# Kernel optimization log

Hardware: AMD Instinct MI355X
Metric: run time of the kernel (lower is better)

Reference implementation:

```python
import jax, jax.numpy as jnp
import numpy as np

B, S, E, H = 4, 4096, 768, 8
D = E // H  # head_dim = 96


def setup_inputs() -> dict:
    key = jax.random.key(0)
    ks = jax.random.split(key, 9)
    std = 1.0 / np.sqrt(E)
    return {
        "values": jax.random.normal(ks[0], (B, S, E), dtype=jnp.float32),
        "keys": jax.random.normal(ks[1], (B, S, E), dtype=jnp.float32),
        "query": jax.random.normal(ks[2], (B, S, E), dtype=jnp.float32),
        "mask": jax.random.randint(ks[3], (B, S, 1, 1), 0, 2, dtype=jnp.int32),
        "Wv": jax.random.normal(ks[4], (E, E), dtype=jnp.float32) * std,
        "Wk": jax.random.normal(ks[5], (E, E), dtype=jnp.float32) * std,
        "Wq": jax.random.normal(ks[6], (E, E), dtype=jnp.float32) * std,
        "Wo": jax.random.normal(ks[7], (E, E), dtype=jnp.float32) * std,
        "bo": jax.random.normal(ks[8], (E,), dtype=jnp.float32) * std,
    }


def reference(values, keys, query, mask, Wv, Wk, Wq, Wo, bo):
    b, s, e = query.shape
    h, d = H, e // H
    scale = e ** 0.5

    def split(x, W):
        # Linear (no bias) then view to [b, s, h, d] and permute to [b, h, s, d]
        return (x @ W.T).reshape(b, s, h, d).transpose(0, 2, 1, 3)

    v = split(values, Wv)   # [b, h, s, d]
    k = split(keys, Wk)     # [b, h, s, d]
    q = split(query, Wq)    # [b, h, s, d]

    # Faithful to torch.einsum('nqhd,nkhd->nhqk', q, k) with q,k laid out as
    # [b, h, s, d]: this contracts over d with s batched, producing a per-token
    # head-gram matrix att[b, s, i, j] = sum_d q[b,i,s,d] * k[b,j,s,d].
    att = jnp.einsum('bisd,bjsd->bsij', q, k)          # [b, s, h, h]
    att = jnp.where(mask == 0, jnp.float32(-1e20), att)
    att = jax.nn.softmax(att / scale, axis=3)

    # torch.einsum('nhql,nlhd->nqhd', att, v) with att [b,s,h,h], v [b,h,s,d]:
    # out[b, i, s, d] = sum_j att[b,s,i,j] * v[b,j,s,d]  -> [b, h, s, d]
    out = jnp.einsum('bsij,bjsd->bisd', att, v)        # [b, h, s, d]
    out = out.reshape(b, s, h * d)                      # row-major, matches torch .reshape
    return out @ Wo.T + bo
```

## Files before the change

### kernel.cpp

```cpp
#include <hip/hip_runtime.h>
#include <hip/hip_bf16.h>
#include <cstdint>


typedef unsigned short u16;
typedef short bf16x8 __attribute__((ext_vector_type(8)));
typedef float f32x4 __attribute__((ext_vector_type(4)));

#define B_  4
#define S_  4096
#define E_  768
#define H_  8
#define D_  96
#define T_  (B_*S_)
#define BM_ 128
#define BN_ 128
#define NT_ (E_/BN_)

static __device__ __forceinline__ u16 f2bf(float f) {
  unsigned u = __builtin_bit_cast(unsigned, f);
  u += 0x7fffu + ((u >> 16) & 1u);
  return (u16)(u >> 16);
}
static __device__ __forceinline__ unsigned pk2(float lo, float hi) {
  return (unsigned)f2bf(lo) | ((unsigned)f2bf(hi) << 16);
}
static __device__ __forceinline__ float bflo(unsigned u) {
  return __builtin_bit_cast(float, u << 16);
}
static __device__ __forceinline__ float bfhi(unsigned u) {
  return __builtin_bit_cast(float, u & 0xffff0000u);
}

__global__ __launch_bounds__(256) void conv_bf16(
    const float* __restrict__ src, u16* __restrict__ dst)
{
  const int i = blockIdx.x * 256 + threadIdx.x;
  const float4 v = ((const float4*)src)[i];
  uint2 w;
  w.x = pk2(v.x, v.y);
  w.y = pk2(v.z, v.w);
  ((uint2*)dst)[i] = w;
}

__global__ __launch_bounds__(256) void conv_w(
    const float* __restrict__ w0, const float* __restrict__ w1,
    const float* __restrict__ w2, const float* __restrict__ w3,
    u16* __restrict__ dst)
{
  const int bpw = (E_ * E_ / 4) / 256;
  const int which = blockIdx.x / bpw;
  const float* src = which == 0 ? w0 : which == 1 ? w1 : which == 2 ? w2 : w3;
  const int i = (blockIdx.x - which * bpw) * 256 + threadIdx.x;
  const float4 v = ((const float4*)src)[i];
  uint2 w;
  w.x = pk2(v.x, v.y);
  w.y = pk2(v.z, v.w);
  ((uint2*)(dst + (size_t)which * E_ * E_))[i] = w;
}

#define STAGE(BUF, KT)                                                         \
  {                                                                            \
    _Pragma("unroll")                                                          \
    for (int c = 0; c < 2; ++c) {                                              \
      const int idx = (c << 8) + tid;                                          \
      const int r = idx >> 2, g = idx & 3;                                     \
      const int gs = g ^ ((r >> 1) & 3);                                       \
      __builtin_amdgcn_global_load_lds(                                        \
          (const __attribute__((address_space(1))) void*)                     \
              (A + (size_t)(tM + r) * E_ + (KT) + (gs << 3)),                  \
          (__attribute__((address_space(3))) void*)                           \
              &lds[BUF][0][((c << 8) + (wave << 6)) << 3], 16, 0, 0);          \
      __builtin_amdgcn_global_load_lds(                                        \
          (const __attribute__((address_space(1))) void*)                     \
              (Wt + (size_t)(tN + r) * E_ + (KT) + (gs << 3)),                 \
          (__attribute__((address_space(3))) void*)                           \
              &lds[BUF][1][((c << 8) + (wave << 6)) << 3], 16, 0, 0);          \
    }                                                                          \
  }

#define LOADFRAGS(BUF)                                                         \
  {                                                                            \
    _Pragma("unroll")                                                          \
    for (int m = 0; m < 4; ++m)                                                \
      a[m] = *(const bf16x8*)&lds[BUF][0][((wr << 6) + (m << 4) + l15) * 32 + slotOff]; \
    _Pragma("unroll")                                                          \
    for (int n = 0; n < 4; ++n)                                                \
      b[n] = *(const bf16x8*)&lds[BUF][1][((wc << 6) + (n << 4) + l15) * 32 + slotOff]; \
  }

#define DOMFMA()                                                               \
  {                                                                            \
    _Pragma("unroll")                                                          \
    for (int m = 0; m < 4; ++m)                                                \
      _Pragma("unroll")                                                        \
      for (int n = 0; n < 4; ++n)                                              \
        acc[m][n] = __builtin_amdgcn_mfma_f32_16x16x32_bf16(a[m], b[n], acc[m][n], 0, 0, 0); \
  }

template<bool OUT_F32, bool BIAS>
__global__ __launch_bounds__(256, 3) void gemm_nt(
    const u16* __restrict__ A, const u16* __restrict__ Wt,
    const float* __restrict__ bias, void* __restrict__ Cv)
{
  __shared__ u16 lds[2][2][BM_ * 32];
  const int tid  = threadIdx.x;
  const int wave = tid >> 6;
  const int lane = tid & 63;
  const int wr = wave >> 1, wc = wave & 1;
  const int bid = blockIdx.x;
  const int wg  = (bid & 7) * (gridDim.x >> 3) + (bid >> 3);
  const int mT  = wg / NT_;
  const int nT  = wg - mT * NT_;
  const int tM = mT * BM_, tN = nT * BN_;
  const int l15 = lane & 15, l4 = lane >> 4;
  const int slotOff = (l4 ^ ((l15 >> 1) & 3)) << 3;

  f32x4 acc[4][4] = {};

  STAGE(0, 0);
  __syncthreads();

  for (int i = 0; i < 12; ++i) {
    const int kt = i << 6;
    {
      bf16x8 a[4], b[4];
      LOADFRAGS(0);
      STAGE(1, kt + 32);
      DOMFMA();
    }
    __syncthreads();
    {
      bf16x8 a[4], b[4];
      LOADFRAGS(1);
      if (i < 11) STAGE(0, kt + 64);
      DOMFMA();
    }
    __syncthreads();
  }

  if constexpr (OUT_F32) {
#pragma unroll
    for (int m = 0; m < 4; ++m) {
#pragma unroll
      for (int n = 0; n < 4; ++n) {
        const int row = tM + (wr << 6) + (m << 4) + (l4 << 2);
        const int col = tN + (wc << 6) + (n << 4) + l15;
        const float badd = BIAS ? bias[col] : 0.f;
#pragma unroll
        for (int r = 0; r < 4; ++r)
          ((float*)Cv)[(size_t)(row + r) * E_ + col] = acc[m][n][r] + badd;
      }
    }
  } else {
    __syncthreads();
    u16* lC = (u16*)lds;
#pragma unroll
    for (int m = 0; m < 4; ++m)
#pragma unroll
      for (int n = 0; n < 4; ++n) {
        const int row = (wr << 6) + (m << 4) + (l4 << 2);
        const int col = (wc << 6) + (n << 4) + l15;
#pragma unroll
        for (int r = 0; r < 4; ++r)
          lC[(row + r) * BN_ + col] = f2bf(acc[m][n][r]);
      }
    __syncthreads();
#pragma unroll
    for (int p = 0; p < 8; ++p) {
      const int row = (p << 4) + (wave << 2) + l4;
      const bf16x8 v = *(const bf16x8*)&lC[row * BN_ + (l15 << 3)];
      *(bf16x8*)((u16*)Cv + (size_t)(tM + row) * E_ + tN + (l15 << 3)) = v;
    }
  }
}

__global__ __launch_bounds__(256) void attn_tok(
    const u16* __restrict__ Q, const u16* __restrict__ K,
    const u16* __restrict__ V, const int* __restrict__ mask,
    u16* __restrict__ O)
{
  __shared__ float pl[4][8][8];
  const int tid = threadIdx.x, wave = tid >> 6, lane = tid & 63;
  const int t = blockIdx.x * 4 + wave;
  const int s = t & (S_ - 1);
  const int b = t >> 12;
  const int i = lane >> 3, j = lane & 7;

  const uint4* qp = (const uint4*)(Q + (size_t)t * E_ + i * D_);
  const uint4* kp = (const uint4*)(K + (size_t)t * E_ + j * D_);
  float acc = 0.f;
#pragma unroll
  for (int it = 0; it < 12; ++it) {
    const uint4 qv = qp[it], kv = kp[it];
    acc += bflo(qv.x) * bflo(kv.x) + bfhi(qv.x) * bfhi(kv.x);
    acc += bflo(qv.y) * bflo(kv.y) + bfhi(qv.y) * bfhi(kv.y);
    acc += bflo(qv.z) * bflo(kv.z) + bfhi(qv.z) * bfhi(kv.z);
    acc += bflo(qv.w) * bflo(kv.w) + bfhi(qv.w) * bfhi(kv.w);
  }
  float sv = (mask[t] == 0) ? -1e20f : acc;
  sv *= 0.03608439182435161f;
  float mx = sv;
  mx = fmaxf(mx, __shfl_xor(mx, 1));
  mx = fmaxf(mx, __shfl_xor(mx, 2));
  mx = fmaxf(mx, __shfl_xor(mx, 4));
  const float e = __expf(sv - mx);
  float sm = e;
  sm += __shfl_xor(sm, 1);
  sm += __shfl_xor(sm, 2);
  sm += __shfl_xor(sm, 4);
  pl[wave][i][j] = e / sm;
  __syncthreads();

  const int i2 = lane >> 3, db = lane & 7;
  float o[12] = {};
#pragma unroll
  for (int jj = 0; jj < 8; ++jj) {
    const float pj = pl[wave][i2][jj];
    const uint2* vp = (const uint2*)(V + (size_t)t * E_ + jj * D_ + db * 12);
    const uint2 v0 = vp[0], v1 = vp[1], v2 = vp[2];
    o[0]  += pj * bflo(v0.x);  o[1]  += pj * bfhi(v0.x);
    o[2]  += pj * bflo(v0.y);  o[3]  += pj * bfhi(v0.y);
    o[4]  += pj * bflo(v1.x);  o[5]  += pj * bfhi(v1.x);
    o[6]  += pj * bflo(v1.y);  o[7]  += pj * bfhi(v1.y);
    o[8]  += pj * bflo(v2.x);  o[9]  += pj * bfhi(v2.x);
    o[10] += pj * bflo(v2.y);  o[11] += pj * bfhi(v2.y);
  }
  const size_t row = (size_t)b * S_ + 512 * i2 + (s >> 3);
  u16* op = O + row * E_ + 96 * (s & 7) + db * 12;
  uint2 w0, w1, w2;
  w0.x = pk2(o[0], o[1]);
  w0.y = pk2(o[2], o[3]);
  w1.x = pk2(o[4], o[5]);
  w1.y = pk2(o[6], o[7]);
  w2.x = pk2(o[8], o[9]);
  w2.y = pk2(o[10], o[11]);
  ((uint2*)op)[0] = w0;
  ((uint2*)op)[1] = w1;
  ((uint2*)op)[2] = w2;
}

extern "C" void kernel_launch(void* const* d_in, const int* in_sizes, int n_in,
                              void* d_out, int out_size, void* d_ws, size_t ws_size,
                              hipStream_t stream)
{
  const float* values = (const float*)d_in[0];
  const float* keys   = (const float*)d_in[1];
  const float* query  = (const float*)d_in[2];
  const int*   mask   = (const int*)d_in[3];
  const float* Wv = (const float*)d_in[4];
  const float* Wk = (const float*)d_in[5];
  const float* Wq = (const float*)d_in[6];
  const float* Wo = (const float*)d_in[7];
  const float* bo = (const float*)d_in[8];

  const size_t TE = (size_t)T_ * E_;
  const size_t EE = (size_t)E_ * E_;
  u16* Qb = (u16*)d_ws;
  u16* Kb = Qb + TE;
  u16* Vb = Kb + TE;
  u16* Xt = Vb + TE;
  u16* Wb = Xt + TE;

  dim3 blk(256);
  dim3 gg(T_ / BM_ * NT_);
  dim3 gc(TE / 4 / 256);

  conv_w<<<dim3(4 * (E_ * E_ / 4) / 256), blk, 0, stream>>>(Wq, Wk, Wv, Wo, Wb);

  conv_bf16<<<gc, blk, 0, stream>>>(query, Xt);
  gemm_nt<false, false><<<gg, blk, 0, stream>>>(Xt, Wb + 0 * EE, nullptr, Qb);
  conv_bf16<<<gc, blk, 0, stream>>>(keys, Xt);
  gemm_nt<false, false><<<gg, blk, 0, stream>>>(Xt, Wb + 1 * EE, nullptr, Kb);
  conv_bf16<<<gc, blk, 0, stream>>>(values, Xt);
  gemm_nt<false, false><<<gg, blk, 0, stream>>>(Xt, Wb + 2 * EE, nullptr, Vb);

  attn_tok<<<dim3(T_ / 4), blk, 0, stream>>>(Qb, Kb, Vb, mask, Xt );

  gemm_nt<true, true><<<gg, blk, 0, stream>>>(Xt , Wb + 3 * EE, bo, (float*)d_out);
}
```

Measured before the change: 194.4 us.

## Fuse fp32-to-bf16 activation conversion into projection GEMM A-tile loading

Removes the three standalone conversion kernels and has the Q/K/V projection GEMMs read the fp32 activations directly. Each thread loads its fp32 values into registers, overlaps the loads with the MFMAs, and then packs them to bf16 with v_cvt_pk_bf16_f32 before writing them into swizzled LDS. This avoids writing and re-reading a bf16 copy of each input plus three extra launches. In exchange, the A tile is fetched at fp32 width through registers instead of via direct global-to-LDS loads, which raises register pressure and global traffic per tile and may change rounding behaviour on edge cases.

After: 227.2 us. 16.9% more time.

```diff
diff --git a/kernel.cpp b/kernel.cpp
--- a/kernel.cpp
+++ b/kernel.cpp
@@ -25,22 +25,16 @@
 static __device__ __forceinline__ unsigned pk2(float lo, float hi) {
   return (unsigned)f2bf(lo) | ((unsigned)f2bf(hi) << 16);
 }
+static __device__ __forceinline__ unsigned cvtpk(float lo, float hi) {
+  unsigned r;
+  asm("v_cvt_pk_bf16_f32 %0, %1, %2" : "=v"(r) : "v"(lo), "v"(hi));
+  return r;
+}
 static __device__ __forceinline__ float bflo(unsigned u) {
   return __builtin_bit_cast(float, u << 16);
 }
 static __device__ __forceinline__ float bfhi(unsigned u) {
   return __builtin_bit_cast(float, u & 0xffff0000u);
-}
-
-__global__ __launch_bounds__(256) void conv_bf16(
-    const float* __restrict__ src, u16* __restrict__ dst)
-{
-  const int i = blockIdx.x * 256 + threadIdx.x;
-  const float4 v = ((const float4*)src)[i];
-  uint2 w;
-  w.x = pk2(v.x, v.y);
-  w.y = pk2(v.z, v.w);
-  ((uint2*)dst)[i] = w;
 }
 
 __global__ __launch_bounds__(256) void conv_w(
@@ -59,7 +53,8 @@
   ((uint2*)(dst + (size_t)which * E_ * E_))[i] = w;
 }
 
-#define STAGE(BUF, KT)                                                         \
+
+#define STAGE_OP(BUF, OP, PTR, TBASE, KT)                                      \
   {                                                                            \
     _Pragma("unroll")                                                          \
     for (int c = 0; c < 2; ++c) {                                              \
@@ -68,15 +63,27 @@
       const int gs = g ^ ((r >> 1) & 3);                                       \
       __builtin_amdgcn_global_load_lds(                                        \
           (const __attribute__((address_space(1))) void*)                     \
-              (A + (size_t)(tM + r) * E_ + (KT) + (gs << 3)),                  \
+              ((PTR) + (size_t)((TBASE) + r) * E_ + (KT) + (gs << 3)),         \
           (__attribute__((address_space(3))) void*)                           \
-              &lds[BUF][0][((c << 8) + (wave << 6)) << 3], 16, 0, 0);          \
-      __builtin_amdgcn_global_load_lds(                                        \
-          (const __attribute__((address_space(1))) void*)                     \
-              (Wt + (size_t)(tN + r) * E_ + (KT) + (gs << 3)),                 \
-          (__attribute__((address_space(3))) void*)                           \
-              &lds[BUF][1][((c << 8) + (wave << 6)) << 3], 16, 0, 0);          \
+              &lds[BUF][OP][((c << 8) + (wave << 6)) << 3], 16, 0, 0);         \
     }                                                                          \
+  }
+
+#define LOAD_A(KT)                                                             \
+  const float4 av0 = *(const float4*)(agp + (KT));                             \
+  const float4 av1 = *(const float4*)(agp + (KT) + 4);                         \
+  const float4 av2 = *(const float4*)(agp + (KT) + 8);                         \
+  const float4 av3 = *(const float4*)(agp + (KT) + 12);
+
+#define WRITE_A(BUF)                                                           \
+  {                                                                            \
+    uint4 q0, q1;                                                              \
+    q0.x = cvtpk(av0.x, av0.y); q0.y = cvtpk(av0.z, av0.w);                    \
+    q0.z = cvtpk(av1.x, av1.y); q0.w = cvtpk(av1.z, av1.w);                    \
+    q1.x = cvtpk(av2.x, av2.y); q1.y = cvtpk(av2.z, av2.w);                    \
+    q1.z = cvtpk(av3.x, av3.y); q1.w = cvtpk(av3.z, av3.w);                    \
+    *(uint4*)&lds[BUF][0][ar * 32 + (((ah << 1) ^ aswz) << 3)] = q0;           \
+    *(uint4*)&lds[BUF][0][ar * 32 + ((((ah << 1) + 1) ^ aswz) << 3)] = q1;     \
   }
 
 #define LOADFRAGS(BUF)                                                         \
@@ -98,9 +105,9 @@
         acc[m][n] = __builtin_amdgcn_mfma_f32_16x16x32_bf16(a[m], b[n], acc[m][n], 0, 0, 0); \
   }
 
-template<bool OUT_F32, bool BIAS>
+template<bool A_F32, bool OUT_F32, bool BIAS>
 __global__ __launch_bounds__(256, 3) void gemm_nt(
-    const u16* __restrict__ A, const u16* __restrict__ Wt,
+    const void* __restrict__ Av, const u16* __restrict__ Wt,
     const float* __restrict__ bias, void* __restrict__ Cv)
 {
   __shared__ u16 lds[2][2][BM_ * 32];
@@ -116,9 +123,22 @@
   const int l15 = lane & 15, l4 = lane >> 4;
   const int slotOff = (l4 ^ ((l15 >> 1) & 3)) << 3;
 
+  const u16*   A16 = (const u16*)Av;
+  const float* A32 = (const float*)Av;
+  const int ar = tid >> 1, ah = tid & 1;
+  const int aswz = (ar >> 1) & 3;
+  const float* agp = A32 + (size_t)(tM + ar) * E_ + ah * 16;
+
   f32x4 acc[4][4] = {};
 
-  STAGE(0, 0);
+  if constexpr (A_F32) {
+    LOAD_A(0);
+    STAGE_OP(0, 1, Wt, tN, 0);
+    WRITE_A(0);
+  } else {
+    STAGE_OP(0, 0, A16, tM, 0);
+    STAGE_OP(0, 1, Wt, tN, 0);
+  }
   __syncthreads();
 
   for (int i = 0; i < 12; ++i) {
@@ -126,15 +146,35 @@
     {
       bf16x8 a[4], b[4];
       LOADFRAGS(0);
-      STAGE(1, kt + 32);
-      DOMFMA();
+      if constexpr (A_F32) {
+        LOAD_A(kt + 32);
+        STAGE_OP(1, 1, Wt, tN, kt + 32);
+        DOMFMA();
+        WRITE_A(1);
+      } else {
+        STAGE_OP(1, 0, A16, tM, kt + 32);
+        STAGE_OP(1, 1, Wt, tN, kt + 32);
+        DOMFMA();
+      }
     }
     __syncthreads();
     {
       bf16x8 a[4], b[4];
       LOADFRAGS(1);
-      if (i < 11) STAGE(0, kt + 64);
-      DOMFMA();
+      if (i < 11) {
+        if constexpr (A_F32) {
+          LOAD_A(kt + 64);
+          STAGE_OP(0, 1, Wt, tN, kt + 64);
+          DOMFMA();
+          WRITE_A(0);
+        } else {
+          STAGE_OP(0, 0, A16, tM, kt + 64);
+          STAGE_OP(0, 1, Wt, tN, kt + 64);
+          DOMFMA();
+        }
+      } else {
+        DOMFMA();
+      }
     }
     __syncthreads();
   }
@@ -259,23 +299,19 @@
   u16* Qb = (u16*)d_ws;
   u16* Kb = Qb + TE;
   u16* Vb = Kb + TE;
-  u16* Xt = Vb + TE;
-  u16* Wb = Xt + TE;
+  u16* O2 = Vb + TE;
+  u16* Wb = O2 + TE;
 
   dim3 blk(256);
   dim3 gg(T_ / BM_ * NT_);
-  dim3 gc(TE / 4 / 256);
 
   conv_w<<<dim3(4 * (E_ * E_ / 4) / 256), blk, 0, stream>>>(Wq, Wk, Wv, Wo, Wb);
 
-  conv_bf16<<<gc, blk, 0, stream>>>(query, Xt);
-  gemm_nt<false, false><<<gg, blk, 0, stream>>>(Xt, Wb + 0 * EE, nullptr, Qb);
-  conv_bf16<<<gc, blk, 0, stream>>>(keys, Xt);
-  gemm_nt<false, false><<<gg, blk, 0, stream>>>(Xt, Wb + 1 * EE, nullptr, Kb);
-  conv_bf16<<<gc, blk, 0, stream>>>(values, Xt);
-  gemm_nt<false, false><<<gg, blk, 0, stream>>>(Xt, Wb + 2 * EE, nullptr, Vb);
-
-  attn_tok<<<dim3(T_ / 4), blk, 0, stream>>>(Qb, Kb, Vb, mask, Xt );
-
-  gemm_nt<true, true><<<gg, blk, 0, stream>>>(Xt , Wb + 3 * EE, bo, (float*)d_out);
-}
+  gemm_nt<true, false, false><<<gg, blk, 0, stream>>>(query,  Wb + 0 * EE, nullptr, Qb);
+  gemm_nt<true, false, false><<<gg, blk, 0, stream>>>(keys,   Wb + 1 * EE, nullptr, Kb);
+  gemm_nt<true, false, false><<<gg, blk, 0, stream>>>(values, Wb + 2 * EE, nullptr, Vb);
+
+  attn_tok<<<dim3(T_ / 4), blk, 0, stream>>>(Qb, Kb, Vb, mask, O2);
+
+  gemm_nt<false, true, true><<<gg, blk, 0, stream>>>(O2, Wb + 3 * EE, bo, (float*)d_out);
+}
```

## Batch QKV conversions and projections into single launches with staggered start

Applied to the files above, without the earlier changes.

Merges the three input bf16 conversions into one kernel and the three Q/K/V projection GEMMs into one launch indexed by blockIdx.y, using the output buffer as scratch for the converted K and V inputs. This removes launch overhead and the serialization of small kernels, and gives the GPU a grid large enough to fill all CUs. It also adds an s_sleep-based stagger so blocks start at different times, which is meant to spread out memory traffic. The stagger adds idle delay at the start of each block, and the swizzle constant is hardcoded to 96.

Result: faster. 175.3 us (-9.8%).

```diff
diff --git a/kernel.cpp b/kernel.cpp
--- a/kernel.cpp
+++ b/kernel.cpp
@@ -32,17 +32,6 @@
   return __builtin_bit_cast(float, u & 0xffff0000u);
 }
 
-__global__ __launch_bounds__(256) void conv_bf16(
-    const float* __restrict__ src, u16* __restrict__ dst)
-{
-  const int i = blockIdx.x * 256 + threadIdx.x;
-  const float4 v = ((const float4*)src)[i];
-  uint2 w;
-  w.x = pk2(v.x, v.y);
-  w.y = pk2(v.z, v.w);
-  ((uint2*)dst)[i] = w;
-}
-
 __global__ __launch_bounds__(256) void conv_w(
     const float* __restrict__ w0, const float* __restrict__ w1,
     const float* __restrict__ w2, const float* __restrict__ w3,
@@ -59,6 +48,28 @@
   ((uint2*)(dst + (size_t)which * E_ * E_))[i] = w;
 }
 
+__global__ __launch_bounds__(256) void conv3(
+    const float* __restrict__ q, const float* __restrict__ k,
+    const float* __restrict__ v, u16* __restrict__ xq,
+    u16* __restrict__ xk, u16* __restrict__ xv)
+{
+  const int w = blockIdx.y;
+  const float* src = w == 0 ? q : w == 1 ? k : v;
+  u16* dst = w == 0 ? xq : w == 1 ? xk : xv;
+  const int i = blockIdx.x * 256 + threadIdx.x;
+  const float4 vv = ((const float4*)src)[i];
+  uint2 o;
+  o.x = pk2(vv.x, vv.y);
+  o.y = pk2(vv.z, vv.w);
+  ((uint2*)dst)[i] = o;
+}
+
+
+#define GLOAD(SRC, DST)                                                        \
+  __builtin_amdgcn_global_load_lds(                                            \
+      (const __attribute__((address_space(1))) void*)(SRC),                    \
+      (__attribute__((address_space(3))) void*)(DST), 16, 0, 0)
+
 #define STAGE(BUF, KT)                                                         \
   {                                                                            \
     _Pragma("unroll")                                                          \
@@ -66,16 +77,10 @@
       const int idx = (c << 8) + tid;                                          \
       const int r = idx >> 2, g = idx & 3;                                     \
       const int gs = g ^ ((r >> 1) & 3);                                       \
-      __builtin_amdgcn_global_load_lds(                                        \
-          (const __attribute__((address_space(1))) void*)                     \
-              (A + (size_t)(tM + r) * E_ + (KT) + (gs << 3)),                  \
-          (__attribute__((address_space(3))) void*)                           \
-              &lds[BUF][0][((c << 8) + (wave << 6)) << 3], 16, 0, 0);          \
-      __builtin_amdgcn_global_load_lds(                                        \
-          (const __attribute__((address_space(1))) void*)                     \
-              (Wt + (size_t)(tN + r) * E_ + (KT) + (gs << 3)),                 \
-          (__attribute__((address_space(3))) void*)                           \
-              &lds[BUF][1][((c << 8) + (wave << 6)) << 3], 16, 0, 0);          \
+      GLOAD(A + (size_t)(tM + r) * E_ + (KT) + (gs << 3),                      \
+            &lds[BUF][0][((c << 8) + (wave << 6)) << 3]);                      \
+      GLOAD(Wt + (size_t)(tN + r) * E_ + (KT) + (gs << 3),                     \
+            &lds[BUF][1][((c << 8) + (wave << 6)) << 3]);                      \
     }                                                                          \
   }
 
@@ -83,10 +88,10 @@
   {                                                                            \
     _Pragma("unroll")                                                          \
     for (int m = 0; m < 4; ++m)                                                \
-      a[m] = *(const bf16x8*)&lds[BUF][0][((wr << 6) + (m << 4) + l15) * 32 + slotOff]; \
+      a[m] = *(const bf16x8*)&lds[BUF][0][(((wr << 6) + (m << 4) + l15) << 5) + slotOff]; \
     _Pragma("unroll")                                                          \
     for (int n = 0; n < 4; ++n)                                                \
-      b[n] = *(const bf16x8*)&lds[BUF][1][((wc << 6) + (n << 4) + l15) * 32 + slotOff]; \
+      b[n] = *(const bf16x8*)&lds[BUF][1][(((wc << 6) + (n << 4) + l15) << 5) + slotOff]; \
   }
 
 #define DOMFMA()                                                               \
@@ -98,18 +103,39 @@
         acc[m][n] = __builtin_amdgcn_mfma_f32_16x16x32_bf16(a[m], b[n], acc[m][n], 0, 0, 0); \
   }
 
-template<bool OUT_F32, bool BIAS>
+template<bool BATCHED, bool OUT_F32, bool BIAS>
 __global__ __launch_bounds__(256, 3) void gemm_nt(
-    const u16* __restrict__ A, const u16* __restrict__ Wt,
-    const float* __restrict__ bias, void* __restrict__ Cv)
-{
-  __shared__ u16 lds[2][2][BM_ * 32];
+    const u16* __restrict__ a0, const u16* __restrict__ a1,
+    const u16* __restrict__ a2, const u16* __restrict__ Wall,
+    const float* __restrict__ bias,
+    void* __restrict__ c0, void* __restrict__ c1, void* __restrict__ c2)
+{
+  __shared__ u16 lds[2][2][4096];
+  const u16* A;
+  const u16* Wt;
+  void* Cv;
+  if constexpr (BATCHED) {
+    const int q_ = blockIdx.y;
+    A  = q_ == 0 ? a0 : q_ == 1 ? a1 : a2;
+    Wt = Wall + (size_t)q_ * (E_ * E_);
+    Cv = q_ == 0 ? c0 : q_ == 1 ? c1 : c2;
+  } else {
+    A = a0; Wt = Wall; Cv = c0;
+  }
+
+  {
+    int sidx = blockIdx.x >> 8;
+    if constexpr (BATCHED) sidx = (sidx + 3 * blockIdx.y) % 5;
+#pragma unroll 1
+    for (int z = 0; z < sidx; ++z) __builtin_amdgcn_s_sleep(3);
+  }
+
   const int tid  = threadIdx.x;
   const int wave = tid >> 6;
   const int lane = tid & 63;
   const int wr = wave >> 1, wc = wave & 1;
   const int bid = blockIdx.x;
-  const int wg  = (bid & 7) * (gridDim.x >> 3) + (bid >> 3);
+  const int wg  = (bid & 7) * 96 + (bid >> 3);
   const int mT  = wg / NT_;
   const int nT  = wg - mT * NT_;
   const int tM = mT * BM_, tN = nT * BN_;
@@ -259,23 +285,22 @@
   u16* Qb = (u16*)d_ws;
   u16* Kb = Qb + TE;
   u16* Vb = Kb + TE;
-  u16* Xt = Vb + TE;
-  u16* Wb = Xt + TE;
+  u16* Xq = Vb + TE;
+  u16* Wb = Xq + TE;
+  u16* Xk = (u16*)d_out;
+  u16* Xv = Xk + TE;
 
   dim3 blk(256);
-  dim3 gg(T_ / BM_ * NT_);
-  dim3 gc(TE / 4 / 256);
 
   conv_w<<<dim3(4 * (E_ * E_ / 4) / 256), blk, 0, stream>>>(Wq, Wk, Wv, Wo, Wb);
 
-  conv_bf16<<<gc, blk, 0, stream>>>(query, Xt);
-  gemm_nt<false, false><<<gg, blk, 0, stream>>>(Xt, Wb + 0 * EE, nullptr, Qb);
-  conv_bf16<<<gc, blk, 0, stream>>>(keys, Xt);
-  gemm_nt<false, false><<<gg, blk, 0, stream>>>(Xt, Wb + 1 * EE, nullptr, Kb);
-  conv_bf16<<<gc, blk, 0, stream>>>(values, Xt);
-  gemm_nt<false, false><<<gg, blk, 0, stream>>>(Xt, Wb + 2 * EE, nullptr, Vb);
-
-  attn_tok<<<dim3(T_ / 4), blk, 0, stream>>>(Qb, Kb, Vb, mask, Xt );
-
-  gemm_nt<true, true><<<gg, blk, 0, stream>>>(Xt , Wb + 3 * EE, bo, (float*)d_out);
-}
+  conv3<<<dim3(TE / 4 / 256, 3), blk, 0, stream>>>(query, keys, values, Xq, Xk, Xv);
+
+  gemm_nt<true, false, false><<<dim3(T_ / BM_ * NT_, 3), blk, 0, stream>>>(
+      Xq, Xk, Xv, Wb, nullptr, Qb, Kb, Vb);
+
+  attn_tok<<<dim3(T_ / 4), blk, 0, stream>>>(Qb, Kb, Vb, mask, Xq );
+
+  gemm_nt<false, true, true><<<dim3(T_ / BM_ * NT_), blk, 0, stream>>>(
+      Xq , nullptr, nullptr, Wb + 3 * EE, bo, (float*)d_out, nullptr, nullptr);
+}
```
